# Kernel optimization log

Measured on AMD Instinct MI355X. Metric: run time of the kernel, lower is better.

## Reference

```python
import jax, jax.numpy as jnp
import numpy as np

H = 256          # hidden_dim from config
B, S = 128, 2048 # batch, seq_len
D_CTX, D_RFX = 6, 2


def setup_inputs() -> dict:
    key = jax.random.key(0)
    ks = jax.random.split(key, 16)
    def lin(k, out_d, in_d):
        # torch nn.Linear default init: U(-1/sqrt(in_d), 1/sqrt(in_d))
        bound = 1.0 / np.sqrt(in_d)
        k1, k2 = jax.random.split(k)
        w = jax.random.uniform(k1, (out_d, in_d), jnp.float32, -bound, bound)
        b = jax.random.uniform(k2, (out_d,), jnp.float32, -bound, bound)
        return w, b
    x = jax.random.normal(ks[0], (B, S, D_CTX), jnp.float32)
    # GRUCell params (torch layout: rows ordered [reset, update, new])
    bnd = 1.0 / np.sqrt(H)
    w_ih = jax.random.uniform(ks[1], (3 * H, D_CTX), jnp.float32, -bnd, bnd)
    w_hh = jax.random.uniform(ks[2], (3 * H, H), jnp.float32, -bnd, bnd)
    b_ih = jax.random.uniform(ks[3], (3 * H,), jnp.float32, -bnd, bnd)
    b_hh = jax.random.uniform(ks[4], (3 * H,), jnp.float32, -bnd, bnd)
    w_gain, b_gain = lin(ks[5], D_RFX, H)
    w_bias, b_bias = lin(ks[6], 4, H)
    w_reflex, b_reflex = lin(ks[7], H, D_RFX)
    w_policy, b_policy = lin(ks[8], 2, H)
    w_motor, b_motor = lin(ks[9], 2, H)
    return dict(x=x, w_ih=w_ih, w_hh=w_hh, b_ih=b_ih, b_hh=b_hh,
                w_gain=w_gain, b_gain=b_gain, w_bias=w_bias, b_bias=b_bias,
                w_reflex=w_reflex, b_reflex=b_reflex,
                w_policy=w_policy, b_policy=b_policy,
                w_motor=w_motor, b_motor=b_motor)


def _forward(x, w_ih, w_hh, b_ih, b_hh, w_gain, b_gain, w_bias, b_bias,
             w_reflex, b_reflex, w_policy, b_policy, w_motor, b_motor):
    # x_context == cat(x[:,:,0:2], x[:,:,2:3], x[:,:,3:6]) == x itself
    x_reflex = x[:, :, 0:2]
    # Precompute input contribution to all 3 GRU gates: [B, S, 3H]
    gates_x = jnp.einsum('bsd,gd->bsg', x, w_ih) + b_ih
    gates_x_t = jnp.swapaxes(gates_x, 0, 1)     # [S, B, 3H]
    x_reflex_t = jnp.swapaxes(x_reflex, 0, 1)   # [S, B, 2]

    h0 = jnp.zeros((x.shape[0], H), x.dtype)

    def step(h, inp):
        gi, xr = inp
        gh = h @ w_hh.T + b_hh
        r = jax.nn.sigmoid(gi[:, :H] + gh[:, :H])
        z = jax.nn.sigmoid(gi[:, H:2 * H] + gh[:, H:2 * H])
        n = jnp.tanh(gi[:, 2 * H:] + r * gh[:, 2 * H:])
        h_new = (1.0 - z) * n + z * h
        gain = jax.nn.sigmoid(h_new @ w_gain.T + b_gain)   # [B,2]
        bias = h_new @ w_bias.T + b_bias                    # [B,4]
        feat = jax.nn.relu((xr * gain) @ w_reflex.T + b_reflex)  # [B,H]
        probs = feat @ w_policy.T + b_policy + bias[:, 0:2]
        dirs = jnp.tanh(feat @ w_motor.T + b_motor + bias[:, 2:4])
        y = jnp.concatenate([probs, dirs], axis=1)          # [B,4]
        return h_new, (y, h_new)

    _, (y_t, h_t) = jax.lax.scan(step, h0, (gates_x_t, x_reflex_t))
    y_pred = jnp.swapaxes(y_t, 0, 1)          # [B,S,4]
    router_activity = jnp.swapaxes(h_t, 0, 1) # [B,S,H]
    return y_pred, router_activity


def reference(x, w_ih, w_hh, b_ih, b_hh, w_gain, b_gain, w_bias, b_bias,
              w_reflex, b_reflex, w_policy, b_policy, w_motor, b_motor):
    return _forward(x, w_ih, w_hh, b_ih, b_hh, w_gain, b_gain, w_bias, b_bias,
                    w_reflex, b_reflex, w_policy, b_policy, w_motor, b_motor)
```

## Files before the change

kernel.cpp:

```cpp
#include <hip/hip_runtime.h>
#include <cstdint>
#include <cstddef>

#define Hn 256
#define Sn 2048
#define Bn 128
#define NT 768

typedef _Float16 half2_t __attribute__((ext_vector_type(2)));

__device__ __forceinline__ float fdot2_(half2_t a, half2_t b, float c){
#if __has_builtin(__builtin_amdgcn_fdot2)
  return __builtin_amdgcn_fdot2(a, b, c, false);
#else
  float d;
  asm volatile("v_dot2_f32_f16 %0, %1, %2, %3" : "=v"(d) : "v"(a), "v"(b), "v"(c));
  return d;
#endif
}

__device__ __forceinline__ float rfl_(float v){
  return __builtin_bit_cast(float, __builtin_amdgcn_readfirstlane(__builtin_bit_cast(int, v)));
}

__device__ __forceinline__ float sigmoid_(float v){ return 1.0f/(1.0f+__expf(-v)); }
__device__ __forceinline__ float tanh_(float v){
  float e = __expf(-2.0f*__builtin_fabsf(v));
  float r = (1.0f-e)/(1.0f+e);
  return __builtin_copysignf(r, v);
}

__global__ void
__attribute__((amdgpu_flat_work_group_size(NT, NT),
               amdgpu_waves_per_eu(3, 3),
               amdgpu_num_vgpr(168)))
bio_rnn(const float* __restrict__ x,
        const float* __restrict__ w_ih, const float* __restrict__ w_hh,
        const float* __restrict__ b_ih, const float* __restrict__ b_hh,
        const float* __restrict__ w_gain, const float* __restrict__ b_gain,
        const float* __restrict__ w_bias, const float* __restrict__ b_bias,
        const float* __restrict__ w_reflex, const float* __restrict__ b_reflex,
        const float* __restrict__ w_policy, const float* __restrict__ b_policy,
        const float* __restrict__ w_motor, const float* __restrict__ b_motor,
        float* __restrict__ y_out, float* __restrict__ router)
{
  const int b = blockIdx.x;
  const int t = threadIdx.x;

  __shared__ __align__(16) half2_t hpk[Hn/2];
  __shared__ float A[NT];
  __shared__ float GIN[Hn];
  __shared__ float REDp[4][8];
  __shared__ float REDq[4][4];
  __shared__ float HW[13][Hn];
  __shared__ float SB[10];

  half2_t w[128];
  {
    const float* wr = w_hh + (size_t)t * Hn;
    #pragma unroll
    for (int k = 0; k < 128; k++){
      half2_t v; v.x = (_Float16)wr[2*k]; v.y = (_Float16)wr[2*k+1];
      w[k] = v;
    }
  }
  half2_t wi0, wi1, wi2;
  {
    const float* wr = w_ih + (size_t)t * 6;
    wi0.x=(_Float16)wr[0]; wi0.y=(_Float16)wr[1];
    wi1.x=(_Float16)wr[2]; wi1.y=(_Float16)wr[3];
    wi2.x=(_Float16)wr[4]; wi2.y=(_Float16)wr[5];
  }
  const float bias_h = b_hh[t];
  const float bias_i = b_ih[t];

  if (t < Hn){
    HW[0][t] = w_gain[t];        HW[1][t]  = w_gain[Hn + t];
    HW[2][t] = w_bias[t];        HW[3][t]  = w_bias[Hn + t];
    HW[4][t] = w_bias[2*Hn + t]; HW[5][t]  = w_bias[3*Hn + t];
    HW[6][t] = w_reflex[2*t];    HW[7][t]  = w_reflex[2*t + 1];
    HW[8][t] = b_reflex[t];
    HW[9][t] = w_policy[t];      HW[10][t] = w_policy[Hn + t];
    HW[11][t] = w_motor[t];      HW[12][t] = w_motor[Hn + t];
  }
  if (t < Hn/2){ half2_t z0; z0.x=(_Float16)0.f; z0.y=(_Float16)0.f; hpk[t] = z0; }
  if (t == 0){
    SB[0]=b_gain[0]; SB[1]=b_gain[1];
    SB[2]=b_bias[0]; SB[3]=b_bias[1]; SB[4]=b_bias[2]; SB[5]=b_bias[3];
    SB[6]=b_policy[0]; SB[7]=b_policy[1]; SB[8]=b_motor[0]; SB[9]=b_motor[1];
  }
  float hprev = 0.f;
  __syncthreads();

  const float* xp = x      + (size_t)b * Sn * 6;
  float* rbase    = router + (size_t)b * Sn * Hn;
  const uint4* hv4 = (const uint4*)hpk;

  for (int s = 0; s < Sn; s++){
    const float x0=rfl_(xp[0]), x1=rfl_(xp[1]), x2=rfl_(xp[2]);
    const float x3=rfl_(xp[3]), x4=rfl_(xp[4]), x5=rfl_(xp[5]);
    half2_t xq0, xq1, xq2;
    xq0.x=(_Float16)x0; xq0.y=(_Float16)x1;
    xq1.x=(_Float16)x2; xq1.y=(_Float16)x3;
    xq2.x=(_Float16)x4; xq2.y=(_Float16)x5;
    float gx = fdot2_(wi2, xq2, fdot2_(wi1, xq1, fdot2_(wi0, xq0, bias_i)));

    float a0 = bias_h, a1 = 0.f, a2 = 0.f, a3 = 0.f;
    #pragma unroll
    for (int k = 0; k < 32; k++){
      uint4 hv = hv4[k];
      a0 = fdot2_(w[4*k+0], __builtin_bit_cast(half2_t, hv.x), a0);
      a1 = fdot2_(w[4*k+1], __builtin_bit_cast(half2_t, hv.y), a1);
      a2 = fdot2_(w[4*k+2], __builtin_bit_cast(half2_t, hv.z), a2);
      a3 = fdot2_(w[4*k+3], __builtin_bit_cast(half2_t, hv.w), a3);
    }
    float acc = (a0 + a1) + (a2 + a3);
    if (t < 512) A[t] = acc + gx;
    else { A[t] = acc; GIN[t - 512] = gx; }
    __syncthreads();

    if (t < Hn){
      float r = sigmoid_(A[t]);
      float z = sigmoid_(A[t + Hn]);
      float n = tanh_(GIN[t] + r * A[t + 2*Hn]);
      float h = (1.f - z) * n + z * hprev;
      hprev = h;
      ((_Float16*)hpk)[t] = (_Float16)h;
      rbase[(size_t)s * Hn + t] = h;
      float p0=h*HW[0][t], p1=h*HW[1][t], p2=h*HW[2][t];
      float p3=h*HW[3][t], p4=h*HW[4][t], p5=h*HW[5][t];
      #pragma unroll
      for (int off = 32; off >= 1; off >>= 1){
        p0 += __shfl_xor(p0, off); p1 += __shfl_xor(p1, off); p2 += __shfl_xor(p2, off);
        p3 += __shfl_xor(p3, off); p4 += __shfl_xor(p4, off); p5 += __shfl_xor(p5, off);
      }
      if ((t & 63) == 0){
        const int wv = t >> 6;
        REDp[wv][0]=p0; REDp[wv][1]=p1; REDp[wv][2]=p2;
        REDp[wv][3]=p3; REDp[wv][4]=p4; REDp[wv][5]=p5;
      }
    }
    __syncthreads();
    if (t < Hn){
      float g0 = REDp[0][0]+REDp[1][0]+REDp[2][0]+REDp[3][0] + SB[0];
      float g1 = REDp[0][1]+REDp[1][1]+REDp[2][1]+REDp[3][1] + SB[1];
      g0 = sigmoid_(g0); g1 = sigmoid_(g1);
      float f = (x0*g0)*HW[6][t] + (x1*g1)*HW[7][t] + HW[8][t];
      f = fmaxf(f, 0.f);
      float q0=f*HW[9][t], q1=f*HW[10][t], q2=f*HW[11][t], q3=f*HW[12][t];
      #pragma unroll
      for (int off = 32; off >= 1; off >>= 1){
        q0 += __shfl_xor(q0, off); q1 += __shfl_xor(q1, off);
        q2 += __shfl_xor(q2, off); q3 += __shfl_xor(q3, off);
      }
      if ((t & 63) == 0){
        const int wv = t >> 6;
        REDq[wv][0]=q0; REDq[wv][1]=q1; REDq[wv][2]=q2; REDq[wv][3]=q3;
      }
    }
    __syncthreads();
    if (t == 0){
      float s0 = REDq[0][0]+REDq[1][0]+REDq[2][0]+REDq[3][0];
      float s1 = REDq[0][1]+REDq[1][1]+REDq[2][1]+REDq[3][1];
      float s2 = REDq[0][2]+REDq[1][2]+REDq[2][2]+REDq[3][2];
      float s3 = REDq[0][3]+REDq[1][3]+REDq[2][3]+REDq[3][3];
      float B0 = REDp[0][2]+REDp[1][2]+REDp[2][2]+REDp[3][2] + SB[2];
      float B1 = REDp[0][3]+REDp[1][3]+REDp[2][3]+REDp[3][3] + SB[3];
      float B2 = REDp[0][4]+REDp[1][4]+REDp[2][4]+REDp[3][4] + SB[4];
      float B3 = REDp[0][5]+REDp[1][5]+REDp[2][5]+REDp[3][5] + SB[5];
      float4 o;
      o.x = s0 + SB[6] + B0;
      o.y = s1 + SB[7] + B1;
      o.z = tanh_(s2 + SB[8] + B2);
      o.w = tanh_(s3 + SB[9] + B3);
      *(float4*)(y_out + (size_t)b * Sn * 4 + (size_t)s * 4) = o;
    }
    xp += 6;
  }
}

extern "C" void kernel_launch(void* const* d_in, const int* in_sizes, int n_in,
                              void* d_out, int out_size, void* d_ws, size_t ws_size,
                              hipStream_t stream)
{
  const float* x        = (const float*)d_in[0];
  const float* w_ih     = (const float*)d_in[1];
  const float* w_hh     = (const float*)d_in[2];
  const float* b_ih     = (const float*)d_in[3];
  const float* b_hh     = (const float*)d_in[4];
  const float* w_gain   = (const float*)d_in[5];
  const float* b_gain   = (const float*)d_in[6];
  const float* w_bias   = (const float*)d_in[7];
  const float* b_bias   = (const float*)d_in[8];
  const float* w_reflex = (const float*)d_in[9];
  const float* b_reflex = (const float*)d_in[10];
  const float* w_policy = (const float*)d_in[11];
  const float* b_policy = (const float*)d_in[12];
  const float* w_motor  = (const float*)d_in[13];
  const float* b_motor  = (const float*)d_in[14];

  float* y_out  = (float*)d_out;
  float* router = (float*)d_out + (size_t)Bn * Sn * 4;

  bio_rnn<<<dim3(Bn), dim3(NT), 0, stream>>>(
      x, w_ih, w_hh, b_ih, b_hh, w_gain, b_gain, w_bias, b_bias,
      w_reflex, b_reflex, w_policy, b_policy, w_motor, b_motor,
      y_out, router);
}
```

Baseline: 6.662 ms.

## Split W_hh across registers, LDS and streamed global loads per step

Each thread now keeps only the first 80 columns of its W_hh row in registers as fp16. The next 80 columns go to LDS, and the last 96 columns are streamed from a pre-converted fp16 workspace every timestep, or from the fp32 weights if the workspace is too small. This lowers VGPR pressure so the fixed 168-VGPR cap and waves_per_eu constraint can be dropped. The cost is extra LDS and global/L2 traffic on every step of the serial recurrence. A separate conversion kernel is launched first to fill the workspace.

```diff
diff --git a/kernel.cpp b/kernel.cpp
--- a/kernel.cpp
+++ b/kernel.cpp
@@ -8,6 +8,10 @@
 #define NT 768
 
 typedef _Float16 half2_t __attribute__((ext_vector_type(2)));
+typedef _Float16 h16 __attribute__((ext_vector_type(16)));
+typedef unsigned int u8v __attribute__((ext_vector_type(8)));
+
+__device__ __forceinline__ half2_t bc2_(unsigned int u){ return __builtin_bit_cast(half2_t, u); }
 
 __device__ __forceinline__ float fdot2_(half2_t a, half2_t b, float c){
 #if __has_builtin(__builtin_amdgcn_fdot2)
@@ -23,6 +27,10 @@
   return __builtin_bit_cast(float, __builtin_amdgcn_readfirstlane(__builtin_bit_cast(int, v)));
 }
 
+__device__ __forceinline__ half2_t pkrtz_(float a, float b){
+  return __builtin_bit_cast(half2_t, __builtin_amdgcn_cvt_pkrtz(a, b));
+}
+
 __device__ __forceinline__ float sigmoid_(float v){ return 1.0f/(1.0f+__expf(-v)); }
 __device__ __forceinline__ float tanh_(float v){
   float e = __expf(-2.0f*__builtin_fabsf(v));
@@ -30,10 +38,18 @@
   return __builtin_copysignf(r, v);
 }
 
-__global__ void
-__attribute__((amdgpu_flat_work_group_size(NT, NT),
-               amdgpu_waves_per_eu(3, 3),
-               amdgpu_num_vgpr(168)))
+__global__ void __launch_bounds__(256)
+cvt_ws(const float* __restrict__ w_hh, unsigned int* __restrict__ ws)
+{
+  int i = blockIdx.x * 256 + threadIdx.x;
+  int row = i / 48, c = i % 48;
+  float f0 = w_hh[(size_t)row*Hn + 160 + 2*c];
+  float f1 = w_hh[(size_t)row*Hn + 160 + 2*c + 1];
+  ws[i] = __builtin_bit_cast(unsigned int, pkrtz_(f0, f1));
+}
+
+template<int SM>
+__global__ void __launch_bounds__(NT)
 bio_rnn(const float* __restrict__ x,
         const float* __restrict__ w_ih, const float* __restrict__ w_hh,
         const float* __restrict__ b_ih, const float* __restrict__ b_hh,
@@ -42,11 +58,13 @@
         const float* __restrict__ w_reflex, const float* __restrict__ b_reflex,
         const float* __restrict__ w_policy, const float* __restrict__ b_policy,
         const float* __restrict__ w_motor, const float* __restrict__ b_motor,
+        const void* __restrict__ wstream,
         float* __restrict__ y_out, float* __restrict__ router)
 {
   const int b = blockIdx.x;
   const int t = threadIdx.x;
 
+  __shared__ unsigned int WL[NT * 44];
   __shared__ __align__(16) half2_t hpk[Hn/2];
   __shared__ float A[NT];
   __shared__ float GIN[Hn];
@@ -55,21 +73,26 @@
   __shared__ float HW[13][Hn];
   __shared__ float SB[10];
 
-  half2_t w[128];
+  h16 W0, W1, W2, W3, W4;
   {
     const float* wr = w_hh + (size_t)t * Hn;
     #pragma unroll
-    for (int k = 0; k < 128; k++){
-      half2_t v; v.x = (_Float16)wr[2*k]; v.y = (_Float16)wr[2*k+1];
-      w[k] = v;
+    for (int i = 0; i < 16; i++){
+      W0[i] = (_Float16)wr[i];       W1[i] = (_Float16)wr[16+i];
+      W2[i] = (_Float16)wr[32+i];    W3[i] = (_Float16)wr[48+i];
+      W4[i] = (_Float16)wr[64+i];
+    }
+    #pragma unroll
+    for (int i = 0; i < 40; i++){
+      WL[t*44 + i] = __builtin_bit_cast(unsigned int, pkrtz_(wr[80+2*i], wr[80+2*i+1]));
     }
   }
   half2_t wi0, wi1, wi2;
   {
     const float* wr = w_ih + (size_t)t * 6;
-    wi0.x=(_Float16)wr[0]; wi0.y=(_Float16)wr[1];
-    wi1.x=(_Float16)wr[2]; wi1.y=(_Float16)wr[3];
-    wi2.x=(_Float16)wr[4]; wi2.y=(_Float16)wr[5];
+    wi0 = pkrtz_(wr[0], wr[1]);
+    wi1 = pkrtz_(wr[2], wr[3]);
+    wi2 = pkrtz_(wr[4], wr[5]);
   }
   const float bias_h = b_hh[t];
   const float bias_i = b_ih[t];
@@ -95,25 +118,73 @@
   const float* xp = x      + (size_t)b * Sn * 6;
   float* rbase    = router + (size_t)b * Sn * Hn;
   const uint4* hv4 = (const uint4*)hpk;
+  const uint4* WLv = (const uint4*)WL;
+  const uint4* S4  = (SM==0) ? ((const uint4*)wstream + (size_t)t*12) : nullptr;
+  const float4* SF = (SM==1) ? ((const float4*)wstream + (size_t)t*64 + 40) : nullptr;
+
+#define DOTG(Wg, hb) { u8v wv = __builtin_bit_cast(u8v, Wg);              \
+    uint4 ha = hv4[hb], hb2 = hv4[(hb)+1];                                 \
+    a0=fdot2_(bc2_(wv[0]),bc2_(ha.x),a0); a1=fdot2_(bc2_(wv[1]),bc2_(ha.y),a1); \
+    a2=fdot2_(bc2_(wv[2]),bc2_(ha.z),a2); a3=fdot2_(bc2_(wv[3]),bc2_(ha.w),a3); \
+    a0=fdot2_(bc2_(wv[4]),bc2_(hb2.x),a0); a1=fdot2_(bc2_(wv[5]),bc2_(hb2.y),a1); \
+    a2=fdot2_(bc2_(wv[6]),bc2_(hb2.z),a2); a3=fdot2_(bc2_(wv[7]),bc2_(hb2.w),a3); }
+
+#define LDOT(c) { uint4 wl = WLv[t*11 + (c)]; uint4 hh = hv4[10 + (c)];    \
+    a0=fdot2_(bc2_(wl.x),bc2_(hh.x),a0); a1=fdot2_(bc2_(wl.y),bc2_(hh.y),a1); \
+    a2=fdot2_(bc2_(wl.z),bc2_(hh.z),a2); a3=fdot2_(bc2_(wl.w),bc2_(hh.w),a3); }
+
+#define SDOT(sv, c) { uint4 hh = hv4[20 + (c)];                            \
+    a0=fdot2_(bc2_(sv.x),bc2_(hh.x),a0); a1=fdot2_(bc2_(sv.y),bc2_(hh.y),a1); \
+    a2=fdot2_(bc2_(sv.z),bc2_(hh.z),a2); a3=fdot2_(bc2_(sv.w),bc2_(hh.w),a3); }
+
+#define SDOTF(sa, sb, c) { uint4 hh = hv4[20 + (c)];                       \
+    half2_t p0 = pkrtz_(sa.x, sa.y);                                       \
+    half2_t p1 = pkrtz_(sa.z, sa.w);                                       \
+    half2_t p2 = pkrtz_(sb.x, sb.y);                                       \
+    half2_t p3 = pkrtz_(sb.z, sb.w);                                       \
+    a0=fdot2_(p0,bc2_(hh.x),a0); a1=fdot2_(p1,bc2_(hh.y),a1);              \
+    a2=fdot2_(p2,bc2_(hh.z),a2); a3=fdot2_(p3,bc2_(hh.w),a3); }
 
   for (int s = 0; s < Sn; s++){
     const float x0=rfl_(xp[0]), x1=rfl_(xp[1]), x2=rfl_(xp[2]);
     const float x3=rfl_(xp[3]), x4=rfl_(xp[4]), x5=rfl_(xp[5]);
-    half2_t xq0, xq1, xq2;
-    xq0.x=(_Float16)x0; xq0.y=(_Float16)x1;
-    xq1.x=(_Float16)x2; xq1.y=(_Float16)x3;
-    xq2.x=(_Float16)x4; xq2.y=(_Float16)x5;
+    half2_t xq0 = pkrtz_(x0, x1);
+    half2_t xq1 = pkrtz_(x2, x3);
+    half2_t xq2 = pkrtz_(x4, x5);
     float gx = fdot2_(wi2, xq2, fdot2_(wi1, xq1, fdot2_(wi0, xq0, bias_i)));
 
     float a0 = bias_h, a1 = 0.f, a2 = 0.f, a3 = 0.f;
-    #pragma unroll
-    for (int k = 0; k < 32; k++){
-      uint4 hv = hv4[k];
-      a0 = fdot2_(w[4*k+0], __builtin_bit_cast(half2_t, hv.x), a0);
-      a1 = fdot2_(w[4*k+1], __builtin_bit_cast(half2_t, hv.y), a1);
-      a2 = fdot2_(w[4*k+2], __builtin_bit_cast(half2_t, hv.z), a2);
-      a3 = fdot2_(w[4*k+3], __builtin_bit_cast(half2_t, hv.w), a3);
-    }
+
+    if (SM == 0){
+      uint4 s0=S4[0], s1=S4[1], s2=S4[2], s3=S4[3];
+      DOTG(W0,0); DOTG(W1,2); DOTG(W2,4);
+      uint4 s4=S4[4], s5=S4[5], s6=S4[6], s7=S4[7];
+      DOTG(W3,6); DOTG(W4,8);
+      LDOT(0); LDOT(1); LDOT(2); LDOT(3); LDOT(4);
+      uint4 s8=S4[8], s9=S4[9], s10=S4[10], s11=S4[11];
+      LDOT(5); LDOT(6); LDOT(7); LDOT(8); LDOT(9);
+      SDOT(s0,0); SDOT(s1,1); SDOT(s2,2); SDOT(s3,3);
+      SDOT(s4,4); SDOT(s5,5); SDOT(s6,6); SDOT(s7,7);
+      SDOT(s8,8); SDOT(s9,9); SDOT(s10,10); SDOT(s11,11);
+    } else {
+      float4 f0=SF[0], f1=SF[1], f2=SF[2], f3=SF[3];
+      DOTG(W0,0); DOTG(W1,2); DOTG(W2,4);
+      float4 f4=SF[4], f5=SF[5], f6=SF[6], f7=SF[7];
+      DOTG(W3,6); DOTG(W4,8);
+      LDOT(0); LDOT(1); LDOT(2); LDOT(3); LDOT(4);
+      float4 f8=SF[8], f9=SF[9], f10=SF[10], f11=SF[11];
+      LDOT(5); LDOT(6); LDOT(7); LDOT(8); LDOT(9);
+      SDOTF(f0,f1,0); SDOTF(f2,f3,1);
+      float4 f12=SF[12], f13=SF[13], f14=SF[14], f15=SF[15];
+      SDOTF(f4,f5,2); SDOTF(f6,f7,3);
+      float4 f16v=SF[16], f17=SF[17], f18=SF[18], f19=SF[19];
+      SDOTF(f8,f9,4); SDOTF(f10,f11,5);
+      float4 f20=SF[20], f21=SF[21], f22=SF[22], f23=SF[23];
+      SDOTF(f12,f13,6); SDOTF(f14,f15,7);
+      SDOTF(f16v,f17,8); SDOTF(f18,f19,9);
+      SDOTF(f20,f21,10); SDOTF(f22,f23,11);
+    }
+
     float acc = (a0 + a1) + (a2 + a3);
     if (t < 512) A[t] = acc + gx;
     else { A[t] = acc; GIN[t - 512] = gx; }
@@ -177,6 +248,10 @@
     }
     xp += 6;
   }
+#undef DOTG
+#undef LDOT
+#undef SDOT
+#undef SDOTF
 }
 
 extern "C" void kernel_launch(void* const* d_in, const int* in_sizes, int n_in,
@@ -202,8 +277,17 @@
   float* y_out  = (float*)d_out;
   float* router = (float*)d_out + (size_t)Bn * Sn * 4;
 
-  bio_rnn<<<dim3(Bn), dim3(NT), 0, stream>>>(
-      x, w_ih, w_hh, b_ih, b_hh, w_gain, b_gain, w_bias, b_bias,
-      w_reflex, b_reflex, w_policy, b_policy, w_motor, b_motor,
-      y_out, router);
-}
+  const size_t ws_need = (size_t)NT * 48 * 4;
+  if (ws_size >= ws_need){
+    cvt_ws<<<dim3(144), dim3(256), 0, stream>>>(w_hh, (unsigned int*)d_ws);
+    bio_rnn<0><<<dim3(Bn), dim3(NT), 0, stream>>>(
+        x, w_ih, w_hh, b_ih, b_hh, w_gain, b_gain, w_bias, b_bias,
+        w_reflex, b_reflex, w_policy, b_policy, w_motor, b_motor,
+        (const void*)d_ws, y_out, router);
+  } else {
+    bio_rnn<1><<<dim3(Bn), dim3(NT), 0, stream>>>(
+        x, w_ih, w_hh, b_ih, b_hh, w_gain, b_gain, w_bias, b_bias,
+        w_reflex, b_reflex, w_policy, b_policy, w_motor, b_motor,
+        (const void*)w_hh, y_out, router);
+  }
+}
```

After: 5.773 ms. -13.4%, faster.
